# Kernel optimization log

Hardware: AMD Instinct MI355X
Metric: run time of the kernel (lower is better)

## Reference

```python
import jax, jax.numpy as jnp
import numpy as np
from jax import lax

D_MODEL = 1024
H = 16
D_K = D_MODEL // H
B = 2
S = 1024


def _conv3x3(x, w, b):
    # x: [B, C_in, S, S], w: [C_out, C_in, 3, 3], b: [C_out]; SAME padding=1
    y = lax.conv_general_dilated(x, w, window_strides=(1, 1),
                                 padding=((1, 1), (1, 1)),
                                 dimension_numbers=("NCHW", "OIHW", "NCHW"))
    return y + b[None, :, None, None]


def setup_inputs() -> dict:
    key = jax.random.key(0)
    ks = jax.random.split(key, 12)
    q = jax.random.normal(ks[0], (B, S, D_MODEL), dtype=jnp.float32)
    k = jax.random.normal(ks[1], (B, S, D_MODEL), dtype=jnp.float32)
    v = jax.random.normal(ks[2], (B, S, D_MODEL), dtype=jnp.float32)
    mask = jax.random.randint(ks[3], (B, S), 0, 2, dtype=jnp.int32)
    prev = jax.random.normal(ks[4], (B, H, S, S), dtype=jnp.float32)
    sc = 1.0 / np.sqrt(D_MODEL)
    Wq = jax.random.normal(ks[5], (D_MODEL, D_MODEL), dtype=jnp.float32) * sc
    Wk = jax.random.normal(ks[6], (D_MODEL, D_MODEL), dtype=jnp.float32) * sc
    Wv = jax.random.normal(ks[7], (D_MODEL, D_MODEL), dtype=jnp.float32) * sc
    Wo = jax.random.normal(ks[8], (D_MODEL, D_MODEL), dtype=jnp.float32) * sc
    csc = 1.0 / np.sqrt(H * 9)
    Wt = jax.random.normal(ks[9], (H, H, 3, 3), dtype=jnp.float32) * csc
    bt = jnp.zeros((H,), dtype=jnp.float32)
    Wa = jax.random.normal(ks[10], (H, 2 * H, 3, 3), dtype=jnp.float32) * csc
    ba = jnp.zeros((H,), dtype=jnp.float32)
    return {"q": q, "k": k, "v": v, "mask": mask,
            "previous_attention_scores": prev,
            "Wq": Wq, "Wk": Wk, "Wv": Wv, "Wo": Wo,
            "Wt": Wt, "bt": bt, "Wa": Wa, "ba": ba}


def reference(q, k, v, mask, previous_attention_scores,
              Wq, Wk, Wv, Wo, Wt, bt, Wa, ba):
    # Linear projections (torch Linear: x @ W.T), reshape to [B, H, S, D_K]
    def split_heads(x):
        return x.reshape(B, S, H, D_K).transpose(0, 2, 1, 3)
    query = split_heads(q @ Wq.T)
    key_ = split_heads(k @ Wk.T)
    value = split_heads(v @ Wv.T)

    # Raw (unscaled) scores: [B, H, S, S]
    M = jnp.einsum("bhsd,bhtd->bhst", query, key_)
    # Transmit conv on previous layer's attention scores (heads = channels)
    Mt = _conv3x3(previous_attention_scores, Wt, bt)
    # Aggregate conv over concatenated [M, Mt]: 2H -> H channels
    Ma = _conv3x3(jnp.concatenate((M, Mt), axis=1), Wa, ba)
    # NOTE: original scales by sqrt(d_model), not sqrt(d_k)
    A = jax.nn.softmax(Ma / jnp.sqrt(jnp.float32(D_MODEL)), axis=-1)
    # NOTE: original applies masked_fill(-1e9) AFTER softmax (faithful)
    A = jnp.where(mask[:, None, None, :] == 0, jnp.float32(-1e9), A)

    ctx = jnp.einsum("bhst,bhtd->bhsd", A, value)  # [B, H, S, D_K]
    ctx = ctx.transpose(0, 2, 1, 3).reshape(B, S, H * D_K)
    out = ctx @ Wo.T
    return out, A
```

## Files before the change

kernel.cpp:

```cpp
#include <hip/hip_runtime.h>

#define B_  2
#define S_  1024
#define H_  16
#define DK_ 64
#define D_  1024

static const size_t BSD  = (size_t)B_ * S_ * D_;
static const size_t BHSS = (size_t)B_ * H_ * S_ * S_;

typedef __attribute__((ext_vector_type(8))) short bf16x8;
typedef __attribute__((ext_vector_type(4))) float floatx4;

__device__ __forceinline__ unsigned short f2bf(float f) {
  unsigned u = __builtin_bit_cast(unsigned, f);
  unsigned r = (u + 0x7FFFu + ((u >> 16) & 1u)) >> 16;
  return (unsigned short)r;
}

__global__ __launch_bounds__(256) void cvt_bf16_kernel(
    const float* __restrict__ src, unsigned short* __restrict__ dst, int n4) {
  int i = (blockIdx.x << 8) + threadIdx.x;
  if (i >= n4) return;
  float4 v = ((const float4*)src)[i];
  ushort4 o;
  o.x = f2bf(v.x); o.y = f2bf(v.y); o.z = f2bf(v.z); o.w = f2bf(v.w);
  ((ushort4*)dst)[i] = o;
}

__global__ __launch_bounds__(256) void gemm_bf16_nt_kernel(
    const unsigned short* __restrict__ A, const unsigned short* __restrict__ Bw,
    void* __restrict__ Cout, int K, int Mcols, int bf16_out,
    const float* __restrict__ corr) {
  __shared__ short As[64 * 40];
  __shared__ short Bs[64 * 40];
  int tid = threadIdx.x;
  int lane = tid & 63, w = tid >> 6;
  int quad = lane >> 4, xn = lane & 15;
  int row0 = blockIdx.y << 6, col0 = blockIdx.x << 6;
  int rw = w & 1, cw = w >> 1;
  int srow = tid >> 2, sk = (tid & 3) << 3;
  const unsigned short* Ap = A + (size_t)(row0 + srow) * K + sk;
  const unsigned short* Bp = Bw + (size_t)(col0 + srow) * K + sk;
  floatx4 acc[2][2] = {};
  for (int k0 = 0; k0 < K; k0 += 32) {
    uint4 av = *(const uint4*)(Ap + k0);
    uint4 bv = *(const uint4*)(Bp + k0);
    *(uint4*)&As[srow * 40 + sk] = av;
    *(uint4*)&Bs[srow * 40 + sk] = bv;
    __syncthreads();
    bf16x8 af[2], bf[2];
#pragma unroll
    for (int rt = 0; rt < 2; ++rt)
      af[rt] = *(const bf16x8*)&As[(rw * 32 + rt * 16 + xn) * 40 + quad * 8];
#pragma unroll
    for (int ct = 0; ct < 2; ++ct)
      bf[ct] = *(const bf16x8*)&Bs[(cw * 32 + ct * 16 + xn) * 40 + quad * 8];
#pragma unroll
    for (int rt = 0; rt < 2; ++rt)
#pragma unroll
      for (int ct = 0; ct < 2; ++ct)
        acc[rt][ct] = __builtin_amdgcn_mfma_f32_16x16x32_bf16(
            af[rt], bf[ct], acc[rt][ct], 0, 0, 0);
    __syncthreads();
  }
#pragma unroll
  for (int rt = 0; rt < 2; ++rt)
#pragma unroll
    for (int ct = 0; ct < 2; ++ct) {
      int colg = col0 + cw * 32 + ct * 16 + xn;
#pragma unroll
      for (int r = 0; r < 4; ++r) {
        int rowg = row0 + rw * 32 + rt * 16 + quad * 4 + r;
        if (bf16_out)
          ((unsigned short*)Cout)[(size_t)rowg * Mcols + colg] = f2bf(acc[rt][ct][r]);
        else {
          float v = acc[rt][ct][r];
          if (corr) v += corr[((rowg >> 10) << 10) + colg];
          ((float*)Cout)[(size_t)rowg * Mcols + colg] = v;
        }
      }
    }
}

__global__ __launch_bounds__(256) void scores_mfma_kernel(
    const unsigned short* __restrict__ Q, const unsigned short* __restrict__ Km,
    unsigned short* __restrict__ Mo) {
  __shared__ short Qs[128 * 72];
  __shared__ short Ks[64 * 72];
  int z = blockIdx.z, b = z >> 4, h = z & 15;
  int col0 = blockIdx.x << 6, row0 = blockIdx.y << 7;
  int tid = threadIdx.x;
  int lane = tid & 63, w = tid >> 6;
  int quad = lane >> 4, xn = lane & 15;
  const unsigned short* Qb = Q + (size_t)b * S_ * D_ + h * DK_;
  const unsigned short* Kb = Km + (size_t)b * S_ * D_ + h * DK_;
  for (int idx = tid; idx < 1024; idx += 256) {
    int r = idx >> 3, k8 = (idx & 7) << 3;
    uint4 v = *(const uint4*)&Qb[(size_t)(row0 + r) * D_ + k8];
    *(uint4*)&Qs[r * 72 + k8] = v;
  }
  for (int idx = tid; idx < 512; idx += 256) {
    int r = idx >> 3, k8 = (idx & 7) << 3;
    uint4 v = *(const uint4*)&Kb[(size_t)(col0 + r) * D_ + k8];
    *(uint4*)&Ks[r * 72 + k8] = v;
  }
  __syncthreads();
  floatx4 acc[2][4] = {};
#pragma unroll
  for (int ks = 0; ks < 2; ++ks) {
    bf16x8 af[2], bf[4];
#pragma unroll
    for (int rt = 0; rt < 2; ++rt)
      af[rt] = *(const bf16x8*)&Qs[(w * 32 + rt * 16 + xn) * 72 + ks * 32 + quad * 8];
#pragma unroll
    for (int ct = 0; ct < 4; ++ct)
      bf[ct] = *(const bf16x8*)&Ks[(ct * 16 + xn) * 72 + ks * 32 + quad * 8];
#pragma unroll
    for (int rt = 0; rt < 2; ++rt)
#pragma unroll
      for (int ct = 0; ct < 4; ++ct)
        acc[rt][ct] = __builtin_amdgcn_mfma_f32_16x16x32_bf16(
            af[rt], bf[ct], acc[rt][ct], 0, 0, 0);
  }
  unsigned short* Mb = Mo + (size_t)z * S_ * S_;
#pragma unroll
  for (int rt = 0; rt < 2; ++rt)
#pragma unroll
    for (int ct = 0; ct < 4; ++ct) {
      int t = col0 + ct * 16 + xn;
#pragma unroll
      for (int r = 0; r < 4; ++r) {
        int s = row0 + w * 32 + rt * 16 + quad * 4 + r;
        Mb[(size_t)s * S_ + t] = f2bf(acc[rt][ct][r]);
      }
    }
}

__global__ __launch_bounds__(256) void repack16b_kernel(
    const unsigned short* __restrict__ src, unsigned short* __restrict__ dst) {
  int x = (blockIdx.x << 8) + threadIdx.x;
  int y = blockIdx.y, b = blockIdx.z;
  const unsigned short* sp = src + ((size_t)b * 16 * S_ + y) * S_ + x;
  unsigned short out[16];
#pragma unroll
  for (int c = 0; c < 16; ++c) out[c] = sp[(size_t)c << 20];
  unsigned short* dp = dst + (((size_t)b * S_ + y) * S_ + x) * 16;
  unsigned wds[8];
#pragma unroll
  for (int i = 0; i < 8; ++i)
    wds[i] = (unsigned)out[2 * i] | ((unsigned)out[2 * i + 1] << 16);
  uint4 v0 = {wds[0], wds[1], wds[2], wds[3]};
  uint4 v1 = {wds[4], wds[5], wds[6], wds[7]};
  *(uint4*)dp = v0;
  *((uint4*)dp + 1) = v1;
}

__global__ __launch_bounds__(256) void repack16_kernel(
    const float* __restrict__ src, unsigned short* __restrict__ dst) {
  int x = (blockIdx.x << 8) + threadIdx.x;
  int y = blockIdx.y, b = blockIdx.z;
  const float* sp = src + ((size_t)b * 16 * S_ + y) * S_ + x;
  unsigned short out[16];
#pragma unroll
  for (int c = 0; c < 16; ++c) out[c] = f2bf(sp[(size_t)c << 20]);
  unsigned short* dp = dst + (((size_t)b * S_ + y) * S_ + x) * 16;
  unsigned wds[8];
#pragma unroll
  for (int i = 0; i < 8; ++i)
    wds[i] = (unsigned)out[2 * i] | ((unsigned)out[2 * i + 1] << 16);
  uint4 v0 = {wds[0], wds[1], wds[2], wds[3]};
  uint4 v1 = {wds[4], wds[5], wds[6], wds[7]};
  *(uint4*)dp = v0;
  *((uint4*)dp + 1) = v1;
}

__global__ __launch_bounds__(256) void conv_t_mfma_kernel(
    const unsigned short* __restrict__ prevT, const float* __restrict__ Wt,
    const float* __restrict__ bt, unsigned short* __restrict__ Mtbf) {
  __shared__ short Xs[10 * 66 * 24];
  int b = blockIdx.z;
  int x0 = blockIdx.x << 6, y0 = blockIdx.y << 3;
  int tid = threadIdx.x;
  int lane = tid & 63, w = tid >> 6;
  int quad = lane >> 4, xn = lane & 15;

  for (int idx = tid; idx < 1320; idx += 256) {
    int y = idx / 132;
    int r = idx - y * 132;
    int px = r >> 1, half = r & 1;
    int gy = y0 + y - 1, gx = x0 + px - 1;
    uint4 val = {0u, 0u, 0u, 0u};
    if ((unsigned)gy < (unsigned)S_ && (unsigned)gx < (unsigned)S_) {
      const unsigned short* sp =
          prevT + (((size_t)b * S_ + gy) * S_ + gx) * 16 + half * 8;
      val = *(const uint4*)sp;
    }
    *(uint4*)&Xs[(y * 66 + px) * 24 + half * 8] = val;
  }

  int m = xn;
  bf16x8 afr[5];
#pragma unroll
  for (int p = 0; p < 5; ++p) {
#pragma unroll
    for (int j = 0; j < 8; ++j) {
      int k = quad * 8 + j;
      int t = 2 * p + (k >> 4);
      float wv = 0.f;
      if (t < 9) wv = Wt[(m * 16 + (k & 15)) * 9 + t];
      afr[p][j] = (short)f2bf(wv);
    }
  }
  int tdy[5], tdx[5];
#pragma unroll
  for (int p = 0; p < 5; ++p) {
    int t = 2 * p + (quad >> 1);
    if (t > 8) t = 8;
    tdy[p] = t / 3;
    tdx[p] = t - tdy[p] * 3;
  }
  float btl[4];
#pragma unroll
  for (int r = 0; r < 4; ++r) btl[r] = bt[quad * 4 + r];

  __syncthreads();

#pragma unroll
  for (int ry = 0; ry < 2; ++ry) {
    int yl = w * 2 + ry;
    int y = y0 + yl;
#pragma unroll
    for (int seg = 0; seg < 4; ++seg) {
      floatx4 acc = {0.f, 0.f, 0.f, 0.f};
#pragma unroll
      for (int p = 0; p < 5; ++p) {
        const short* bp =
            &Xs[((yl + tdy[p]) * 66 + seg * 16 + xn + tdx[p]) * 24 + (quad & 1) * 8];
        bf16x8 bfr = *(const bf16x8*)bp;
        acc = __builtin_amdgcn_mfma_f32_16x16x32_bf16(afr[p], bfr, acc, 0, 0, 0);
      }
      ushort4 pk;
      pk.x = f2bf(acc[0] + btl[0]);
      pk.y = f2bf(acc[1] + btl[1]);
      pk.z = f2bf(acc[2] + btl[2]);
      pk.w = f2bf(acc[3] + btl[3]);
      int gx = x0 + seg * 16 + xn;
      *(ushort4*)&Mtbf[(((size_t)b * S_ + y) * S_ + gx) * 16 + quad * 4] = pk;
    }
  }
}

__global__ __launch_bounds__(256) void conv_a_softmax_kernel(
    const unsigned short* __restrict__ Mbf, const unsigned short* __restrict__ Mtbf,
    const float* __restrict__ Wa, const float* __restrict__ ba,
    const int* __restrict__ mask,
    float* __restrict__ Aout, unsigned short* __restrict__ P0) {
  __shared__ __attribute__((aligned(16))) short Xs[3 * 132 * 40];
  __shared__ float redm[4][4][4];
  __shared__ float reds[4][4][4];
  int y = ((blockIdx.x & 7) << 7) + (blockIdx.x >> 3);
  int b = blockIdx.y;
  int tid = threadIdx.x;
  int lane = tid & 63, w = tid >> 6;
  int quad = lane >> 4, xn = lane & 15;

  bf16x8 afr[9];
#pragma unroll
  for (int t = 0; t < 9; ++t)
#pragma unroll
    for (int j = 0; j < 8; ++j)
      afr[t][j] = (short)f2bf(Wa[(xn * 32 + quad * 8 + j) * 9 + t]);
  float bal[4];
#pragma unroll
  for (int r = 0; r < 4; ++r) bal[r] = ba[quad * 4 + r];

  floatx4 acc[8][2] = {};
#pragma unroll
  for (int ci = 0; ci < 8; ++ci) {
    int x0 = ci << 7;
    for (int idx = tid; idx < 1560; idx += 256) {
      int ry = idx / 520;
      int rem = idx - ry * 520;
      int px = rem >> 2, part = rem & 3;
      int gy = y + ry - 1, gx = x0 + px - 1;
      uint4 val = {0u, 0u, 0u, 0u};
      if ((unsigned)gy < (unsigned)S_ && (unsigned)gx < (unsigned)S_) {
        const unsigned short* base = (part < 2) ? Mbf : Mtbf;
        val = *(const uint4*)&base[(((size_t)b * S_ + gy) * S_ + gx) * 16 + (part & 1) * 8];
      }
      *(uint4*)&Xs[(ry * 132 + px) * 40 + part * 8] = val;
    }
    __syncthreads();
#pragma unroll
    for (int sub = 0; sub < 2; ++sub) {
      int sp = (w * 2 + sub) * 16 + xn;
      floatx4 a = acc[ci][sub];
#pragma unroll
      for (int t = 0; t < 9; ++t) {
        const int dy = t / 3, dx = t - (t / 3) * 3;
        bf16x8 bfr = *(const bf16x8*)&Xs[(dy * 132 + sp + dx) * 40 + quad * 8];
        a = __builtin_amdgcn_mfma_f32_16x16x32_bf16(afr[t], bfr, a, 0, 0, 0);
      }
      acc[ci][sub] = a;
    }
    __syncthreads();
  }

  const float sc = 1.0f / 32.0f;
  float mx[4] = {-3.4e38f, -3.4e38f, -3.4e38f, -3.4e38f};
#pragma unroll
  for (int ci = 0; ci < 8; ++ci)
#pragma unroll
    for (int sub = 0; sub < 2; ++sub)
#pragma unroll
      for (int r = 0; r < 4; ++r) {
        float v = (acc[ci][sub][r] + bal[r]) * sc;
        acc[ci][sub][r] = v;
        mx[r] = fmaxf(mx[r], v);
      }
#pragma unroll
  for (int r = 0; r < 4; ++r) {
    mx[r] = fmaxf(mx[r], __shfl_xor(mx[r], 1));
    mx[r] = fmaxf(mx[r], __shfl_xor(mx[r], 2));
    mx[r] = fmaxf(mx[r], __shfl_xor(mx[r], 4));
    mx[r] = fmaxf(mx[r], __shfl_xor(mx[r], 8));
  }
  if (xn == 0) {
#pragma unroll
    for (int r = 0; r < 4; ++r) redm[w][quad][r] = mx[r];
  }
  __syncthreads();
  float fm[4];
#pragma unroll
  for (int r = 0; r < 4; ++r)
    fm[r] = fmaxf(fmaxf(redm[0][quad][r], redm[1][quad][r]),
                  fmaxf(redm[2][quad][r], redm[3][quad][r]));
  float sm[4] = {0.f, 0.f, 0.f, 0.f};
#pragma unroll
  for (int ci = 0; ci < 8; ++ci)
#pragma unroll
    for (int sub = 0; sub < 2; ++sub)
#pragma unroll
      for (int r = 0; r < 4; ++r) {
        float e = __expf(acc[ci][sub][r] - fm[r]);
        acc[ci][sub][r] = e;
        sm[r] += e;
      }
#pragma unroll
  for (int r = 0; r < 4; ++r) {
    sm[r] += __shfl_xor(sm[r], 1);
    sm[r] += __shfl_xor(sm[r], 2);
    sm[r] += __shfl_xor(sm[r], 4);
    sm[r] += __shfl_xor(sm[r], 8);
  }
  if (xn == 0) {
#pragma unroll
    for (int r = 0; r < 4; ++r) reds[w][quad][r] = sm[r];
  }
  __syncthreads();
  float inv[4];
#pragma unroll
  for (int r = 0; r < 4; ++r)
    inv[r] = 1.0f / (reds[0][quad][r] + reds[1][quad][r] +
                     reds[2][quad][r] + reds[3][quad][r]);

  const int* mb = mask + b * S_;
#pragma unroll
  for (int ci = 0; ci < 8; ++ci)
#pragma unroll
    for (int sub = 0; sub < 2; ++sub) {
      int gx = (ci << 7) + (w * 2 + sub) * 16 + xn;
      int mk = mb[gx];
#pragma unroll
      for (int r = 0; r < 4; ++r) {
        int mo = quad * 4 + r;
        size_t oidx = (((size_t)(b * 16 + mo)) << 20) + ((size_t)y << 10) + gx;
        float p = acc[ci][sub][r] * inv[r];
        Aout[oidx] = mk ? p : -1e9f;
        P0[oidx]  = mk ? f2bf(p) : (unsigned short)0;
      }
    }
}

__global__ __launch_bounds__(256) void vtrans_kernel(
    const float* __restrict__ V, unsigned short* __restrict__ Vt) {
  __shared__ unsigned short Ls[64][68];
  int z = blockIdx.y, b = z >> 4, h = z & 15;
  int t0 = blockIdx.x << 6;
  int tid = threadIdx.x;
  for (int idx = tid; idx < 1024; idx += 256) {
    int t = idx >> 4, d = (idx & 15) << 2;
    float4 v4 = *(const float4*)&V[((size_t)b * S_ + t0 + t) * D_ + h * 64 + d];
    ushort4 u;
    u.x = f2bf(v4.x); u.y = f2bf(v4.y); u.z = f2bf(v4.z); u.w = f2bf(v4.w);
    *(ushort4*)&Ls[t][d] = u;
  }
  __syncthreads();
  for (int idx = tid; idx < 1024; idx += 256) {
    int d = idx >> 4, tc = (idx & 15) << 2;
    ushort4 u;
    u.x = Ls[tc + 0][d]; u.y = Ls[tc + 1][d];
    u.z = Ls[tc + 2][d]; u.w = Ls[tc + 3][d];
    *(ushort4*)&Vt[((size_t)(h * 64 + d)) * 2048 + (size_t)b * S_ + t0 + tc] = u;
  }
}

__global__ __launch_bounds__(256) void colsum_part_kernel(
    const float* __restrict__ V, const int* __restrict__ mask,
    float* __restrict__ cs_part) {
  int b = blockIdx.z, c = blockIdx.y;
  int d = (blockIdx.x << 8) + threadIdx.x;
  const int* mb = mask + b * S_ + c * 32;
  const float* vp = V + ((size_t)b * S_ + c * 32) * D_ + d;
  float s = 0.f;
#pragma unroll
  for (int i = 0; i < 32; ++i) {
    float vv = vp[(size_t)i * D_];
    if (mb[i] == 0) s += vv;
  }
  cs_part[((size_t)b * 32 + c) * D_ + d] = s;
}

__global__ __launch_bounds__(256) void colsum_reduce_kernel(
    const float* __restrict__ cs_part, float* __restrict__ cs) {
  int i = (blockIdx.x << 8) + threadIdx.x;
  int b = i >> 10, d = i & 1023;
  const float* pp = cs_part + ((size_t)b * 32) * D_ + d;
  float s = 0.f;
#pragma unroll
  for (int c = 0; c < 32; ++c) s += pp[(size_t)c * D_];
  cs[i] = s;
}

__global__ __launch_bounds__(256) void corr_kernel(
    const float* __restrict__ cs, const float* __restrict__ Wo,
    float* __restrict__ corr) {
  int b = blockIdx.y;
  int j = (blockIdx.x << 6) + (threadIdx.x >> 2);
  int part = threadIdx.x & 3;
  const float* c = cs + b * D_ + part * 256;
  const float* wr = Wo + (size_t)j * D_ + part * 256;
  float s = 0.f;
  for (int i = 0; i < 256; i += 4) {
    float4 w4 = *(const float4*)&wr[i];
    float4 c4 = *(const float4*)&c[i];
    s = fmaf(w4.x, c4.x, s); s = fmaf(w4.y, c4.y, s);
    s = fmaf(w4.z, c4.z, s); s = fmaf(w4.w, c4.w, s);
  }
  s += __shfl_xor(s, 1);
  s += __shfl_xor(s, 2);
  if (part == 0) corr[b * D_ + j] = -1e9f * s;
}

__global__ __launch_bounds__(256) void ctx_mfma_kernel(
    const unsigned short* __restrict__ P0, const unsigned short* __restrict__ Vt,
    unsigned short* __restrict__ Cbf) {
  __shared__ __attribute__((aligned(16))) short Ps[64 * 72];
  __shared__ __attribute__((aligned(16))) short Vs[64 * 72];
  int z = blockIdx.y, b = z >> 4, h = z & 15;
  int row0 = blockIdx.x << 6;
  int tid = threadIdx.x, lane = tid & 63, w = tid >> 6;
  int quad = lane >> 4, xn = lane & 15;
  const unsigned short* Pb = P0 + (size_t)z * S_ * S_ + (size_t)row0 * S_;
  const unsigned short* Vb = Vt + ((size_t)h * 64) * 2048 + (size_t)b * S_;
  floatx4 acc[4] = {};
  for (int k0 = 0; k0 < S_; k0 += 64) {
    for (int idx = tid; idx < 512; idx += 256) {
      int r = idx >> 3, c = (idx & 7) << 3;
      *(uint4*)&Ps[r * 72 + c] = *(const uint4*)&Pb[(size_t)r * S_ + k0 + c];
    }
    for (int idx = tid; idx < 512; idx += 256) {
      int r = idx >> 3, c = (idx & 7) << 3;
      *(uint4*)&Vs[r * 72 + c] = *(const uint4*)&Vb[(size_t)r * 2048 + k0 + c];
    }
    __syncthreads();
#pragma unroll
    for (int ks = 0; ks < 2; ++ks) {
      bf16x8 af = *(const bf16x8*)&Ps[(w * 16 + xn) * 72 + ks * 32 + quad * 8];
#pragma unroll
      for (int ct = 0; ct < 4; ++ct) {
        bf16x8 bfv = *(const bf16x8*)&Vs[(ct * 16 + xn) * 72 + ks * 32 + quad * 8];
        acc[ct] = __builtin_amdgcn_mfma_f32_16x16x32_bf16(af, bfv, acc[ct], 0, 0, 0);
      }
    }
    __syncthreads();
  }
  unsigned short* Co = Cbf + ((size_t)b * S_) * D_ + h * 64;
#pragma unroll
  for (int ct = 0; ct < 4; ++ct)
#pragma unroll
    for (int r = 0; r < 4; ++r) {
      int s = row0 + w * 16 + quad * 4 + r;
      Co[(size_t)s * D_ + ct * 16 + xn] = f2bf(acc[ct][r]);
    }
}

extern "C" void kernel_launch(void* const* d_in, const int* in_sizes, int n_in,
                              void* d_out, int out_size, void* d_ws, size_t ws_size,
                              hipStream_t stream) {
  const float* q    = (const float*)d_in[0];
  const float* k    = (const float*)d_in[1];
  const float* v    = (const float*)d_in[2];
  const int*   mask = (const int*)d_in[3];
  const float* prev = (const float*)d_in[4];
  const float* Wq   = (const float*)d_in[5];
  const float* Wk   = (const float*)d_in[6];
  const float* Wv   = (const float*)d_in[7];
  const float* Wo   = (const float*)d_in[8];
  const float* Wt   = (const float*)d_in[9];
  const float* bt   = (const float*)d_in[10];
  const float* Wa   = (const float*)d_in[11];
  const float* ba   = (const float*)d_in[12];

  float* out0 = (float*)d_out;
  float* Aout = out0 + BSD;

  char* wsp = (char*)d_ws;
  unsigned short* X1   = (unsigned short*)wsp; wsp += BSD * 2;
  unsigned short* W1   = (unsigned short*)wsp; wsp += (size_t)D_ * D_ * 2;
  unsigned short* Qb   = (unsigned short*)wsp; wsp += BSD * 2;
  unsigned short* Kb   = (unsigned short*)wsp; wsp += BSD * 2;
  float* Vb            = (float*)wsp;          wsp += BSD * 4;
  unsigned short* Vtb  = (unsigned short*)wsp; wsp += BSD * 2;
  unsigned short* ctx1 = (unsigned short*)wsp; wsp += BSD * 2;
  float* cs            = (float*)wsp;          wsp += (size_t)B_ * D_ * 4;
  float* corrb         = (float*)wsp;          wsp += (size_t)B_ * D_ * 4;
  float* cs_part       = (float*)wsp;          wsp += (size_t)B_ * 32 * D_ * 4;
  unsigned short* Mp   = (unsigned short*)wsp; wsp += BHSS * 2;
  unsigned short* Mbf  = (unsigned short*)wsp; wsp += BHSS * 2;
  unsigned short* Mtbf = (unsigned short*)wsp; wsp += BHSS * 2;
  unsigned short* prevT = Mp;
  unsigned short* P0    = Mp;

  dim3 blk(256);
  int n4x = (int)(BSD / 4);
  int n4w = (D_ * D_) / 4;
  dim3 gX((n4x + 255) / 256), gW((n4w + 255) / 256);
  dim3 gProjB(D_ / 64, (B_ * S_) / 64);

  hipLaunchKernelGGL(cvt_bf16_kernel, gW, blk, 0, stream, Wq, W1, n4w);
  hipLaunchKernelGGL(cvt_bf16_kernel, gX, blk, 0, stream, q, X1, n4x);
  hipLaunchKernelGGL(gemm_bf16_nt_kernel, gProjB, blk, 0, stream, X1, W1,
                     (void*)Qb, D_, D_, 1, (const float*)nullptr);
  hipLaunchKernelGGL(cvt_bf16_kernel, gW, blk, 0, stream, Wk, W1, n4w);
  hipLaunchKernelGGL(cvt_bf16_kernel, gX, blk, 0, stream, k, X1, n4x);
  hipLaunchKernelGGL(gemm_bf16_nt_kernel, gProjB, blk, 0, stream, X1, W1,
                     (void*)Kb, D_, D_, 1, (const float*)nullptr);
  hipLaunchKernelGGL(cvt_bf16_kernel, gW, blk, 0, stream, Wv, W1, n4w);
  hipLaunchKernelGGL(cvt_bf16_kernel, gX, blk, 0, stream, v, X1, n4x);
  hipLaunchKernelGGL(gemm_bf16_nt_kernel, gProjB, blk, 0, stream, X1, W1,
                     (void*)Vb, D_, D_, 0, (const float*)nullptr);
  hipLaunchKernelGGL(cvt_bf16_kernel, gW, blk, 0, stream, Wo, W1, n4w);

  hipLaunchKernelGGL(vtrans_kernel, dim3(S_ / 64, B_ * H_), blk, 0, stream, Vb, Vtb);
  hipLaunchKernelGGL(colsum_part_kernel, dim3(D_ / 256, 32, B_), blk, 0, stream,
                     Vb, mask, cs_part);
  hipLaunchKernelGGL(colsum_reduce_kernel, dim3((B_ * D_) / 256), blk, 0, stream,
                     cs_part, cs);
  hipLaunchKernelGGL(corr_kernel, dim3(D_ / 64, B_), blk, 0, stream, cs, Wo, corrb);

  dim3 gSc(S_ / 64, S_ / 128, B_ * H_);
  hipLaunchKernelGGL(scores_mfma_kernel, gSc, blk, 0, stream, Qb, Kb, Mp);

  dim3 gRep(S_ / 256, S_, B_);
  hipLaunchKernelGGL(repack16b_kernel, gRep, blk, 0, stream, Mp, Mbf);

  hipLaunchKernelGGL(repack16_kernel, gRep, blk, 0, stream, prev, prevT);

  dim3 gConv(S_ / 64, S_ / 8, B_);
  hipLaunchKernelGGL(conv_t_mfma_kernel, gConv, blk, 0, stream, prevT, Wt, bt, Mtbf);

  hipLaunchKernelGGL(conv_a_softmax_kernel, dim3(S_, B_), blk, 0, stream,
                     Mbf, Mtbf, Wa, ba, mask, Aout, P0);

  hipLaunchKernelGGL(ctx_mfma_kernel, dim3(S_ / 64, B_ * H_), blk, 0, stream,
                     P0, Vtb, ctx1);

  dim3 gProj(D_ / 64, (B_ * S_) / 64);
  hipLaunchKernelGGL(gemm_bf16_nt_kernel, gProj, blk, 0, stream, ctx1, W1,
                     (void*)out0, D_, D_, 0, (const float*)corrb);
}
```

Before: 677.7 us.

## Give each wave a private halo tile in conv_a to drop block barriers

The conv_a+softmax kernel used to load a shared 3x132 halo tile per 128-column chunk, with two block-wide __syncthreads per chunk. Now each wave loads its own 3x34 halo tile for its 32 columns and synchronises only with wave barriers. This removes block-level stalls and the divide/modulo index arithmetic in the load loop. In exchange, each wave reloads two halo columns that neighbouring waves also load, so there is more redundant global traffic, and LDS use grows slightly.

```diff
diff --git a/kernel.cpp b/kernel.cpp
--- a/kernel.cpp
+++ b/kernel.cpp
@@ -256,7 +256,7 @@
     const float* __restrict__ Wa, const float* __restrict__ ba,
     const int* __restrict__ mask,
     float* __restrict__ Aout, unsigned short* __restrict__ P0) {
-  __shared__ __attribute__((aligned(16))) short Xs[3 * 132 * 40];
+  __shared__ __attribute__((aligned(16))) short Xs[4 * 3 * 34 * 40];
   __shared__ float redm[4][4][4];
   __shared__ float reds[4][4][4];
   int y = ((blockIdx.x & 7) << 7) + (blockIdx.x >> 3);
@@ -275,36 +275,52 @@
 #pragma unroll
   for (int r = 0; r < 4; ++r) bal[r] = ba[quad * 4 + r];
 
+  short* XsW = &Xs[w * (3 * 34 * 40)];
+
+  int px4 = lane >> 2, part = lane & 3;
+  const unsigned short* rowp[3];
+  int vy[3];
+#pragma unroll
+  for (int ry = 0; ry < 3; ++ry) {
+    int gy = y + ry - 1;
+    vy[ry] = ((unsigned)gy < (unsigned)S_) ? 1 : 0;
+    int gyc = vy[ry] ? gy : 0;
+    const unsigned short* base = (part < 2) ? Mbf : Mtbf;
+    rowp[ry] = base + ((size_t)b * S_ + gyc) * (S_ * 16) + (part & 1) * 8;
+  }
+
   floatx4 acc[8][2] = {};
 #pragma unroll
   for (int ci = 0; ci < 8; ++ci) {
-    int x0 = ci << 7;
-    for (int idx = tid; idx < 1560; idx += 256) {
-      int ry = idx / 520;
-      int rem = idx - ry * 520;
-      int px = rem >> 2, part = rem & 3;
-      int gy = y + ry - 1, gx = x0 + px - 1;
-      uint4 val = {0u, 0u, 0u, 0u};
-      if ((unsigned)gy < (unsigned)S_ && (unsigned)gx < (unsigned)S_) {
-        const unsigned short* base = (part < 2) ? Mbf : Mtbf;
-        val = *(const uint4*)&base[(((size_t)b * S_ + gy) * S_ + gx) * 16 + (part & 1) * 8];
-      }
-      *(uint4*)&Xs[(ry * 132 + px) * 40 + part * 8] = val;
-    }
-    __syncthreads();
+    int x0 = (ci << 7) + (w << 5);
+#pragma unroll
+    for (int ry = 0; ry < 3; ++ry) {
+#pragma unroll
+      for (int g = 0; g < 3; ++g) {
+        if (g < 2 || px4 < 2) {
+          int px = (g << 4) + px4;
+          int gx = x0 + px - 1;
+          uint4 val = {0u, 0u, 0u, 0u};
+          if (vy[ry] && (unsigned)gx < (unsigned)S_)
+            val = *(const uint4*)(rowp[ry] + (size_t)gx * 16);
+          *(uint4*)&XsW[(ry * 34 + px) * 40 + part * 8] = val;
+        }
+      }
+    }
+    __builtin_amdgcn_wave_barrier();
 #pragma unroll
     for (int sub = 0; sub < 2; ++sub) {
-      int sp = (w * 2 + sub) * 16 + xn;
+      int sp = (sub << 4) + xn;
       floatx4 a = acc[ci][sub];
 #pragma unroll
       for (int t = 0; t < 9; ++t) {
         const int dy = t / 3, dx = t - (t / 3) * 3;
-        bf16x8 bfr = *(const bf16x8*)&Xs[(dy * 132 + sp + dx) * 40 + quad * 8];
+        bf16x8 bfr = *(const bf16x8*)&XsW[(dy * 34 + sp + dx) * 40 + quad * 8];
         a = __builtin_amdgcn_mfma_f32_16x16x32_bf16(afr[t], bfr, a, 0, 0, 0);
       }
       acc[ci][sub] = a;
     }
-    __syncthreads();
+    __builtin_amdgcn_wave_barrier();
   }
 
   const float sc = 1.0f / 32.0f;
@@ -370,7 +386,7 @@
   for (int ci = 0; ci < 8; ++ci)
 #pragma unroll
     for (int sub = 0; sub < 2; ++sub) {
-      int gx = (ci << 7) + (w * 2 + sub) * 16 + xn;
+      int gx = (ci << 7) + (w << 5) + (sub << 4) + xn;
       int mk = mb[gx];
 #pragma unroll
       for (int r = 0; r < 4; ++r) {
```

New measurement: 675.9 us. No clear change (-0.3%).
